# Performance work log

Measured on AMD Instinct MI355X. Metric: run time of the kernel, lower is better.

## Reference

```python
import jax, jax.numpy as jnp
import numpy as np

B, S, D, H = 4, 4096, 1024, 16
DH = D // H  # 64
EPS = 1e-6


def setup_inputs() -> dict:
    key = jax.random.key(0)
    ks = jax.random.split(key, 6)
    scale = 1.0 / np.sqrt(D).astype(np.float32)
    x = jax.random.normal(ks[0], (B, S, D), jnp.float32)
    # packed cache: rows 0..DH-1 = KV state S0, row DH = normalizer z0 (kept positive)
    state_cache = jax.random.uniform(ks[1], (B, H, DH + 1, DH), jnp.float32)
    Wq = jax.random.normal(ks[2], (D, D), jnp.float32) * scale
    Wk = jax.random.normal(ks[3], (D, D), jnp.float32) * scale
    Wv = jax.random.normal(ks[4], (D, D), jnp.float32) * scale
    Wo = jax.random.normal(ks[5], (D, D), jnp.float32) * scale
    return {"x": x, "state_cache": state_cache, "Wq": Wq, "Wk": Wk, "Wv": Wv, "Wo": Wo}


def reference(x, state_cache, Wq, Wk, Wv, Wo):
    b, s, d = x.shape
    h, dh = H, d // H

    def heads(t):  # [b,s,d] -> [s,b,h,dh] (seq-major for scan)
        return t.reshape(b, s, h, dh).transpose(1, 0, 2, 3)

    phi = lambda t: jax.nn.elu(t) + 1.0  # positive feature map
    q = phi(heads(x @ Wq))
    k = phi(heads(x @ Wk))
    v = heads(x @ Wv)

    S0 = state_cache[:, :, :dh, :]   # [b,h,dh,dh]
    z0 = state_cache[:, :, dh, :]    # [b,h,dh]

    def step(carry, inp):
        Sst, z = carry
        qt, kt, vt = inp  # each [b,h,dh]
        Sst = Sst + jnp.einsum('bhd,bhe->bhde', kt, vt)
        z = z + kt
        num = jnp.einsum('bhd,bhde->bhe', qt, Sst)            # [b,h,dh]
        den = jnp.einsum('bhd,bhd->bh', qt, z)[..., None]     # [b,h,1]
        return (Sst, z), num / (den + EPS)

    _, outs = jax.lax.scan(step, (S0, z0), (q, k, v))  # outs: [s,b,h,dh]
    out = outs.transpose(1, 0, 2, 3).reshape(b, s, d)
    return out @ Wo
```

## Files before the change

### kernel.cpp

```cpp
#include <hip/hip_runtime.h>

#define B_ 4
#define S_ 4096
#define D_ 1024
#define H_ 16
#define DH 64
#define CHUNK 64
#define NC (S_ / CHUNK)
#define BH (B_ * H_)
#define EPS 1e-6f

typedef __bf16 bf16;
typedef __bf16 bf16x8 __attribute__((ext_vector_type(8)));
typedef __bf16 bf16x4 __attribute__((ext_vector_type(4)));
typedef float v4f __attribute__((ext_vector_type(4)));

#define MFMA16(a, b, c) __builtin_amdgcn_mfma_f32_16x16x32_bf16(a, b, c, 0, 0, 0)

__device__ __forceinline__ void load_lds16(const bf16* g, bf16* l) {
  __builtin_amdgcn_global_load_lds(
      (const __attribute__((address_space(1))) unsigned int*)g,
      (__attribute__((address_space(3))) unsigned int*)l, 16, 0, 0);
}

__device__ __forceinline__ int swz72(int row, int col) {
  return row * 72 + ((((col >> 3) ^ (row >> 3)) & 7) << 3) + (col & 7);
}

__global__ __launch_bounds__(256) void cvt_f32_bf16(const float* __restrict__ in,
                                                    bf16* __restrict__ out) {
  const size_t i = ((size_t)blockIdx.x * 256 + threadIdx.x) * 8;
  float4 a = *(const float4*)(in + i);
  float4 b = *(const float4*)(in + i + 4);
  bf16x8 o;
  o[0] = (bf16)a.x; o[1] = (bf16)a.y; o[2] = (bf16)a.z; o[3] = (bf16)a.w;
  o[4] = (bf16)b.x; o[5] = (bf16)b.y; o[6] = (bf16)b.z; o[7] = (bf16)b.w;
  *(bf16x8*)(out + i) = o;
}

__global__ __launch_bounds__(256) void transpose_w4(
    const float* __restrict__ w0, const float* __restrict__ w1,
    const float* __restrict__ w2, const float* __restrict__ w3,
    bf16* __restrict__ out) {
  __shared__ float tile[32][33];
  const int z = blockIdx.z;
  const float* in = (z == 0) ? w0 : (z == 1) ? w1 : (z == 2) ? w2 : w3;
  bf16* o = out + (size_t)z * D_ * D_;
  const int bx = blockIdx.x * 32, by = blockIdx.y * 32;
  const int tx = threadIdx.x & 31, ty = threadIdx.x >> 5;
#pragma unroll
  for (int i = 0; i < 32; i += 8)
    tile[ty + i][tx] = in[(size_t)(by + ty + i) * D_ + bx + tx];
  __syncthreads();
#pragma unroll
  for (int i = 0; i < 32; i += 8)
    o[(size_t)(bx + ty + i) * D_ + by + tx] = (bf16)tile[tx][ty + i];
}

__global__ __launch_bounds__(256) void gemm_nt(const bf16* __restrict__ A,
                                               const bf16* __restrict__ BT,
                                               bf16* __restrict__ o0,
                                               bf16* __restrict__ o1,
                                               bf16* __restrict__ o2,
                                               float* __restrict__ of) {
  constexpr int TM = 128, BK = 32;
  constexpr int CLD = 132;
  __shared__ __align__(16) char smem[32768];
  float* Cl = (float*)smem;

  const int tid = threadIdx.x;
  const int wave = tid >> 6, lane = tid & 63;
  const int quad = lane >> 4, l16 = lane & 15;
  const int bm = blockIdx.x * TM;
  const int zz = blockIdx.y >> 3;
  const int colg = (blockIdx.y & 7) * 128;
  const int wm = (wave & 1) * 64, wn = (wave >> 1) * 64;
  const int act = (of == nullptr) && (zz < 2);
  bf16* ob = (zz == 0) ? o0 : (zz == 1) ? o1 : o2;

  const int srow = wave * 16 + (lane >> 2);
  const int sgrp = ((lane & 3) - ((lane >> 2) >> 1)) & 3;
  const bf16* gA0 = A + (size_t)(bm + srow) * D_ + sgrp * 8;
  const bf16* gA1 = gA0 + (size_t)64 * D_;
  const bf16* gB0 = BT + ((size_t)blockIdx.y * 128 + srow) * D_ + sgrp * 8;
  const bf16* gB1 = gB0 + (size_t)64 * D_;

  int offA[4], offB[4];
#pragma unroll
  for (int i = 0; i < 4; i++) {
    const int pg = (quad + (l16 >> 1)) & 3;
    offA[i] = (wm + i * 16 + l16) * BK + pg * 8;
    offB[i] = (wn + i * 16 + l16) * BK + pg * 8;
  }

  v4f zero = {0.f, 0.f, 0.f, 0.f};
  v4f acc[4][4];
#pragma unroll
  for (int i = 0; i < 4; i++)
#pragma unroll
    for (int j = 0; j < 4; j++) acc[i][j] = zero;

  auto stage = [&](int ks, int s) {
    bf16* As = (bf16*)(smem + s * 16384);
    bf16* Bs = As + 4096;
    const int ko = ks * BK;
    load_lds16(gA0 + ko, As + wave * 16 * BK);
    load_lds16(gA1 + ko, As + (64 + wave * 16) * BK);
    load_lds16(gB0 + ko, Bs + wave * 16 * BK);
    load_lds16(gB1 + ko, Bs + (64 + wave * 16) * BK);
  };
  auto compute = [&](int s) {
    const bf16* As = (const bf16*)(smem + s * 16384);
    const bf16* Bs = As + 4096;
    bf16x8 af[4], bfr[4];
#pragma unroll
    for (int i = 0; i < 4; i++) af[i] = *(const bf16x8*)&As[offA[i]];
#pragma unroll
    for (int j = 0; j < 4; j++) bfr[j] = *(const bf16x8*)&Bs[offB[j]];
#pragma unroll
    for (int i = 0; i < 4; i++)
#pragma unroll
      for (int j = 0; j < 4; j++) acc[i][j] = MFMA16(af[i], bfr[j], acc[i][j]);
  };

  constexpr int NK = D_ / BK;
  stage(0, 0);
  __syncthreads();
  for (int k = 0; k < NK; k += 2) {
    if (k + 1 < NK) stage(k + 1, 1);
    compute(0);
    __syncthreads();
    if (k + 2 < NK) stage(k + 2, 0);
    compute(1);
    __syncthreads();
  }

  const int lr = (wave & 1) * 16 + quad * 4;
  const int rrow = tid >> 3;
  const int rseg = (tid & 7) * 16;
  const int grow = bm + (rrow >> 4) * 64 + (rrow & 15);
#pragma unroll
  for (int i = 0; i < 4; i++) {
    __syncthreads();
#pragma unroll
    for (int j = 0; j < 4; j++) {
      const int col = wn + j * 16 + l16;
#pragma unroll
      for (int r = 0; r < 4; r++) {
        float x = acc[i][j][r];
        if (act) x = x > 0.f ? x + 1.f : __expf(x);
        Cl[(lr + r) * CLD + col] = x;
      }
    }
    __syncthreads();
    const float* src = &Cl[rrow * CLD + rseg];
    if (of) {
      float* dst = of + (size_t)(grow + i * 16) * D_ + colg + rseg;
#pragma unroll
      for (int u = 0; u < 4; u++)
        *(float4*)(dst + u * 4) = *(const float4*)(src + u * 4);
    } else {
      bf16x8 q0, q1;
#pragma unroll
      for (int u = 0; u < 8; u++) { q0[u] = (bf16)src[u]; q1[u] = (bf16)src[8 + u]; }
      bf16* dst = ob + (size_t)(grow + i * 16) * D_ + colg + rseg;
      *(bf16x8*)dst = q0;
      *(bf16x8*)(dst + 8) = q1;
    }
  }
}

__global__ __launch_bounds__(256) void chunk_kv(const bf16* __restrict__ kb,
                                                const bf16* __restrict__ vb,
                                                bf16* __restrict__ csum,
                                                float* __restrict__ zbuf) {
  __shared__ __align__(16) bf16 KT[DH * 72];
  __shared__ __align__(16) bf16 VT[DH * 72];
  const int tid = threadIdx.x;
  const int wave = tid >> 6, lane = tid & 63;
  const int quad = lane >> 4, l16 = lane & 15;
  const int c = blockIdx.x, bh = blockIdx.y;
  const int b = bh >> 4, h = bh & 15;
  const size_t gbase = ((size_t)(b * S_ + c * CHUNK)) * D_ + h * DH;
#pragma unroll
  for (int rep = 0; rep < 2; rep++) {
    int flat = tid + rep * 256;
    int r = flat >> 3, sg = (flat & 7) * 8;
    bf16x8 kk = *(const bf16x8*)(kb + gbase + (size_t)r * D_ + sg);
    bf16x8 vv = *(const bf16x8*)(vb + gbase + (size_t)r * D_ + sg);
#pragma unroll
    for (int u = 0; u < 8; u++) {
      KT[swz72(sg + u, r)] = kk[u];
      VT[swz72(sg + u, r)] = vv[u];
    }
  }
  __syncthreads();

  v4f zero = {0.f, 0.f, 0.f, 0.f};
  v4f acc[4];
#pragma unroll
  for (int j = 0; j < 4; j++) acc[j] = zero;
#pragma unroll
  for (int ks = 0; ks < 2; ks++) {
    bf16x8 ak = *(const bf16x8*)&KT[swz72(wave * 16 + l16, ks * 32 + quad * 8)];
#pragma unroll
    for (int j = 0; j < 4; j++) {
      bf16x8 bv = *(const bf16x8*)&VT[swz72(j * 16 + l16, ks * 32 + quad * 8)];
      acc[j] = MFMA16(ak, bv, acc[j]);
    }
  }
  bf16* out = csum + ((size_t)bh * NC + c) * 4096;
#pragma unroll
  for (int j = 0; j < 4; j++)
#pragma unroll
    for (int r = 0; r < 4; r++)
      out[(wave * 16 + quad * 4 + r) * 64 + (j * 16 + l16)] = (bf16)acc[j][r];

  {
    const int d = tid >> 2, p = tid & 3;
    bf16x8 a0 = *(const bf16x8*)&KT[swz72(d, p * 16)];
    bf16x8 a1 = *(const bf16x8*)&KT[swz72(d, p * 16 + 8)];
    float zp = 0.f;
#pragma unroll
    for (int u = 0; u < 8; u++) zp += (float)a0[u] + (float)a1[u];
    zp += __shfl_xor(zp, 1, 64);
    zp += __shfl_xor(zp, 2, 64);
    if (p == 0) zbuf[((size_t)bh * NC + c) * 64 + d] = zp;
  }
}

__global__ __launch_bounds__(256) void state_prefix(const float* __restrict__ sc,
                                                    const bf16* __restrict__ csum,
                                                    float* __restrict__ zbuf,
                                                    bf16* __restrict__ stb) {
  const int bh = blockIdx.x;
  const int e = blockIdx.y * 256 + threadIdx.x;
  const float* scb = sc + (size_t)bh * (DH + 1) * DH;
  if (e < 4096) {
    float run = scb[e];
    const bf16* p = csum + (size_t)bh * NC * 4096 + e;
    bf16* q = stb + (size_t)bh * NC * 4096 + e;
#pragma unroll 1
    for (int c = 0; c < NC; c += 4) {
      float t0 = (float)p[(size_t)(c + 0) * 4096];
      float t1 = (float)p[(size_t)(c + 1) * 4096];
      float t2 = (float)p[(size_t)(c + 2) * 4096];
      float t3 = (float)p[(size_t)(c + 3) * 4096];
      q[(size_t)(c + 0) * 4096] = (bf16)run; run += t0;
      q[(size_t)(c + 1) * 4096] = (bf16)run; run += t1;
      q[(size_t)(c + 2) * 4096] = (bf16)run; run += t2;
      q[(size_t)(c + 3) * 4096] = (bf16)run; run += t3;
    }
  } else if (e < 4160) {
    const int d = e - 4096;
    float run = scb[4096 + d];
    float* p = zbuf + (size_t)bh * NC * 64 + d;
#pragma unroll 1
    for (int c = 0; c < NC; c += 4) {
      float t0 = p[(size_t)(c + 0) * 64];
      float t1 = p[(size_t)(c + 1) * 64];
      float t2 = p[(size_t)(c + 2) * 64];
      float t3 = p[(size_t)(c + 3) * 64];
      p[(size_t)(c + 0) * 64] = run; run += t0;
      p[(size_t)(c + 1) * 64] = run; run += t1;
      p[(size_t)(c + 2) * 64] = run; run += t2;
      p[(size_t)(c + 3) * 64] = run; run += t3;
    }
  }
}

__global__ __launch_bounds__(256) void attn_pass2(
    const bf16* __restrict__ qb, const bf16* __restrict__ kb,
    const bf16* __restrict__ vb, const float* __restrict__ zbuf,
    const bf16* __restrict__ stb, bf16* __restrict__ ao) {
  __shared__ __align__(16) bf16 Ql[CHUNK * 72];
  __shared__ __align__(16) bf16 Kl[CHUNK * 72];
  __shared__ __align__(16) bf16 VT[DH * 72];
  __shared__ __align__(16) bf16 S0T[DH * 72];
  __shared__ __align__(16) bf16 Pl[CHUNK * 72];
  __shared__ float denl[CHUNK];
  __shared__ float z0l[DH];
  const int tid = threadIdx.x;
  const int wave = tid >> 6, lane = tid & 63;
  const int quad = lane >> 4, l16 = lane & 15;
  const int c = blockIdx.x, bh = blockIdx.y;
  const int b = bh >> 4, h = bh & 15;
  const size_t gbase = ((size_t)(b * S_ + c * CHUNK)) * D_ + h * DH;

#pragma unroll
  for (int rep = 0; rep < 2; rep++) {
    int flat = tid + rep * 256;
    int r = flat >> 3, sg = (flat & 7) * 8;
    *(bf16x8*)&Ql[swz72(r, sg)] = *(const bf16x8*)(qb + gbase + (size_t)r * D_ + sg);
    *(bf16x8*)&Kl[swz72(r, sg)] = *(const bf16x8*)(kb + gbase + (size_t)r * D_ + sg);
    bf16x8 vv = *(const bf16x8*)(vb + gbase + (size_t)r * D_ + sg);
#pragma unroll
    for (int u = 0; u < 8; u++) VT[swz72(sg + u, r)] = vv[u];
  }
  {
    const bf16* stb_c = stb + ((size_t)bh * NC + c) * 4096;
    const int f0 = tid * 16;
    const int col = f0 >> 6, row0 = f0 & 63;
    bf16x8 a0 = *(const bf16x8*)&stb_c[f0];
    bf16x8 a1 = *(const bf16x8*)&stb_c[f0 + 8];
#pragma unroll
    for (int u = 0; u < 8; u++) {
      S0T[swz72(row0 + u, col)] = a0[u];
      S0T[swz72(row0 + 8 + u, col)] = a1[u];
    }
  }
  if (tid < DH) z0l[tid] = zbuf[((size_t)bh * NC + c) * 64 + tid];
  __syncthreads();

  v4f zero = {0.f, 0.f, 0.f, 0.f};
  v4f pacc[4];
#pragma unroll
  for (int j = 0; j < 4; j++) pacc[j] = zero;
#pragma unroll
  for (int ks = 0; ks < 2; ks++) {
    bf16x8 aq = *(const bf16x8*)&Ql[swz72(wave * 16 + l16, ks * 32 + quad * 8)];
#pragma unroll
    for (int j = 0; j < 4; j++) {
      bf16x8 bk = *(const bf16x8*)&Kl[swz72(j * 16 + l16, ks * 32 + quad * 8)];
      pacc[j] = MFMA16(aq, bk, pacc[j]);
    }
  }
  float rs[4] = {0.f, 0.f, 0.f, 0.f};
#pragma unroll
  for (int j = 0; j < 4; j++) {
#pragma unroll
    for (int r = 0; r < 4; r++) {
      int t = wave * 16 + quad * 4 + r;
      int col = j * 16 + l16;
      float p = (col <= t) ? pacc[j][r] : 0.f;
      Pl[swz72(t, col)] = (bf16)p;
      rs[r] += p;
    }
  }
#pragma unroll
  for (int m = 1; m < 16; m <<= 1)
#pragma unroll
    for (int r = 0; r < 4; r++) rs[r] += __shfl_xor(rs[r], m, 64);
  if (l16 == 0)
#pragma unroll
    for (int r = 0; r < 4; r++) denl[wave * 16 + quad * 4 + r] = rs[r];
  __syncthreads();
  {
    const int t = tid >> 2, p = tid & 3;
    bf16x8 qa = *(const bf16x8*)&Ql[swz72(t, p * 16)];
    bf16x8 qb2 = *(const bf16x8*)&Ql[swz72(t, p * 16 + 8)];
    float qz = 0.f;
#pragma unroll
    for (int u = 0; u < 8; u++)
      qz += (float)qa[u] * z0l[p * 16 + u] + (float)qb2[u] * z0l[p * 16 + 8 + u];
    qz += __shfl_xor(qz, 1, 64);
    qz += __shfl_xor(qz, 2, 64);
    if (p == 0) denl[t] += qz;
  }
  __syncthreads();

  v4f nacc[4];
#pragma unroll
  for (int j = 0; j < 4; j++) nacc[j] = zero;
#pragma unroll
  for (int ks = 0; ks < 2; ks++) {
    bf16x8 ap = *(const bf16x8*)&Pl[swz72(wave * 16 + l16, ks * 32 + quad * 8)];
#pragma unroll
    for (int j = 0; j < 4; j++) {
      bf16x8 bv = *(const bf16x8*)&VT[swz72(j * 16 + l16, ks * 32 + quad * 8)];
      nacc[j] = MFMA16(ap, bv, nacc[j]);
    }
  }
#pragma unroll
  for (int ks = 0; ks < 2; ks++) {
    bf16x8 aq = *(const bf16x8*)&Ql[swz72(wave * 16 + l16, ks * 32 + quad * 8)];
#pragma unroll
    for (int j = 0; j < 4; j++) {
      bf16x8 bs = *(const bf16x8*)&S0T[swz72(j * 16 + l16, ks * 32 + quad * 8)];
      nacc[j] = MFMA16(aq, bs, nacc[j]);
    }
  }

  __syncthreads();
  bf16* Ol = Ql;
#pragma unroll
  for (int j = 0; j < 4; j++) {
#pragma unroll
    for (int r = 0; r < 4; r++) {
      int t = wave * 16 + quad * 4 + r;
      int e = j * 16 + l16;
      Ol[swz72(t, e)] = (bf16)(nacc[j][r] / (denl[t] + EPS));
    }
  }
  __syncthreads();
  {
    const int orow = tid >> 2, oc0 = (tid & 3) * 16;
    bf16x8 q0 = *(const bf16x8*)&Ol[swz72(orow, oc0)];
    bf16x8 q1 = *(const bf16x8*)&Ol[swz72(orow, oc0 + 8)];
    bf16* dst = ao + gbase + (size_t)orow * D_ + oc0;
    *(bf16x8*)dst = q0;
    *(bf16x8*)(dst + 8) = q1;
  }
}

extern "C" void kernel_launch(void* const* d_in, const int* in_sizes, int n_in,
                              void* d_out, int out_size, void* d_ws, size_t ws_size,
                              hipStream_t stream) {
  const float* x  = (const float*)d_in[0];
  const float* sc = (const float*)d_in[1];
  const float* Wq = (const float*)d_in[2];
  const float* Wk = (const float*)d_in[3];
  const float* Wv = (const float*)d_in[4];
  const float* Wo = (const float*)d_in[5];
  float* out = (float*)d_out;

  const size_t MSZ = (size_t)B_ * S_ * D_;
  const size_t WSZ = (size_t)D_ * D_;
  bf16* xb = (bf16*)d_ws;
  bf16* qb = xb + MSZ;
  bf16* kb = qb + MSZ;
  bf16* vb = kb + MSZ;
  bf16* ao = vb + MSZ;
  bf16* wt = ao + MSZ;
  bf16* csum = wt + 4 * WSZ;
  float* zbuf = (float*)(csum + (size_t)BH * NC * 4096);
  bf16* stb = xb;

  cvt_f32_bf16<<<MSZ / (256 * 8), 256, 0, stream>>>(x, xb);
  transpose_w4<<<dim3(32, 32, 4), 256, 0, stream>>>(Wq, Wk, Wv, Wo, wt);

  gemm_nt<<<dim3(128, 24), 256, 0, stream>>>(xb, wt, qb, kb, vb, nullptr);

  chunk_kv<<<dim3(NC, BH), 256, 0, stream>>>(kb, vb, csum, zbuf);
  state_prefix<<<dim3(BH, 17), 256, 0, stream>>>(sc, csum, zbuf, stb);
  attn_pass2<<<dim3(NC, BH), 256, 0, stream>>>(qb, kb, vb, zbuf, stb, ao);

  gemm_nt<<<dim3(128, 8), 256, 0, stream>>>(ao, wt + 3 * WSZ, nullptr, nullptr,
                                            nullptr, out);
}
```

Baseline: 387.6 us.

## Parallelize state prefix scan across chunks with LDS-tiled block scan

The chunk-state prefix kernel previously had each thread walk serially over all 64 chunks for one state element, using only 17 blocks per head with strided scalar bf16 loads. It now launches 64 blocks per head, each loading a 64-column by 64-chunk tile into shared memory with 16-byte vector loads. Four waves each scan 16 chunks, and their partial sums are combined in shared memory. Results are written back with vector stores, and the normalizer scan stays serial in a dedicated extra block. This exposes more parallelism and coalesces memory access, at the cost of extra synchronisation and shared memory.

```diff
diff --git a/kernel.cpp b/kernel.cpp
--- a/kernel.cpp
+++ b/kernel.cpp
@@ -12,7 +12,6 @@
 
 typedef __bf16 bf16;
 typedef __bf16 bf16x8 __attribute__((ext_vector_type(8)));
-typedef __bf16 bf16x4 __attribute__((ext_vector_type(4)));
 typedef float v4f __attribute__((ext_vector_type(4)));
 
 #define MFMA16(a, b, c) __builtin_amdgcn_mfma_f32_16x16x32_bf16(a, b, c, 0, 0, 0)
@@ -234,38 +233,60 @@
                                                     float* __restrict__ zbuf,
                                                     bf16* __restrict__ stb) {
   const int bh = blockIdx.x;
-  const int e = blockIdx.y * 256 + threadIdx.x;
+  const int g = blockIdx.y;
+  const int tid = threadIdx.x;
   const float* scb = sc + (size_t)bh * (DH + 1) * DH;
-  if (e < 4096) {
-    float run = scb[e];
-    const bf16* p = csum + (size_t)bh * NC * 4096 + e;
-    bf16* q = stb + (size_t)bh * NC * 4096 + e;
+  if (g == 64) {
+    if (tid < DH) {
+      const int d = tid;
+      float run = scb[4096 + d];
+      float* p = zbuf + (size_t)bh * NC * 64 + d;
 #pragma unroll 1
-    for (int c = 0; c < NC; c += 4) {
-      float t0 = (float)p[(size_t)(c + 0) * 4096];
-      float t1 = (float)p[(size_t)(c + 1) * 4096];
-      float t2 = (float)p[(size_t)(c + 2) * 4096];
-      float t3 = (float)p[(size_t)(c + 3) * 4096];
-      q[(size_t)(c + 0) * 4096] = (bf16)run; run += t0;
-      q[(size_t)(c + 1) * 4096] = (bf16)run; run += t1;
-      q[(size_t)(c + 2) * 4096] = (bf16)run; run += t2;
-      q[(size_t)(c + 3) * 4096] = (bf16)run; run += t3;
-    }
-  } else if (e < 4160) {
-    const int d = e - 4096;
-    float run = scb[4096 + d];
-    float* p = zbuf + (size_t)bh * NC * 64 + d;
-#pragma unroll 1
-    for (int c = 0; c < NC; c += 4) {
-      float t0 = p[(size_t)(c + 0) * 64];
-      float t1 = p[(size_t)(c + 1) * 64];
-      float t2 = p[(size_t)(c + 2) * 64];
-      float t3 = p[(size_t)(c + 3) * 64];
-      p[(size_t)(c + 0) * 64] = run; run += t0;
-      p[(size_t)(c + 1) * 64] = run; run += t1;
-      p[(size_t)(c + 2) * 64] = run; run += t2;
-      p[(size_t)(c + 3) * 64] = run; run += t3;
-    }
+      for (int c = 0; c < NC; c += 4) {
+        float t0 = p[(size_t)(c + 0) * 64];
+        float t1 = p[(size_t)(c + 1) * 64];
+        float t2 = p[(size_t)(c + 2) * 64];
+        float t3 = p[(size_t)(c + 3) * 64];
+        p[(size_t)(c + 0) * 64] = run; run += t0;
+        p[(size_t)(c + 1) * 64] = run; run += t1;
+        p[(size_t)(c + 2) * 64] = run; run += t2;
+        p[(size_t)(c + 3) * 64] = run; run += t3;
+      }
+    }
+    return;
+  }
+  __shared__ bf16 tile[NC][64];
+  __shared__ bf16 otile[NC][64];
+  __shared__ float partial[4][64];
+  const int x0 = g * 64;
+  const bf16* base = csum + (size_t)bh * NC * 4096 + x0;
+#pragma unroll
+  for (int rep = 0; rep < 2; rep++) {
+    int flat = tid + rep * 256;
+    int c = flat >> 3, seg = (flat & 7) * 8;
+    *(bf16x8*)&tile[c][seg] = *(const bf16x8*)(base + (size_t)c * 4096 + seg);
+  }
+  __syncthreads();
+  const int x = tid & 63, cq = tid >> 6, c0 = cq * 16;
+  float v[16];
+  float s = 0.f;
+#pragma unroll
+  for (int k = 0; k < 16; k++) { v[k] = (float)tile[c0 + k][x]; s += v[k]; }
+  partial[cq][x] = s;
+  __syncthreads();
+  float run = scb[x0 + x];
+#pragma unroll
+  for (int q = 0; q < 3; q++)
+    if (q < cq) run += partial[q][x];
+#pragma unroll
+  for (int k = 0; k < 16; k++) { otile[c0 + k][x] = (bf16)run; run += v[k]; }
+  __syncthreads();
+  bf16* obase = stb + (size_t)bh * NC * 4096 + x0;
+#pragma unroll
+  for (int rep = 0; rep < 2; rep++) {
+    int flat = tid + rep * 256;
+    int c = flat >> 3, seg = (flat & 7) * 8;
+    *(bf16x8*)(obase + (size_t)c * 4096 + seg) = *(const bf16x8*)&otile[c][seg];
   }
 }
 
@@ -432,7 +453,7 @@
   gemm_nt<<<dim3(128, 24), 256, 0, stream>>>(xb, wt, qb, kb, vb, nullptr);
 
   chunk_kv<<<dim3(NC, BH), 256, 0, stream>>>(kb, vb, csum, zbuf);
-  state_prefix<<<dim3(BH, 17), 256, 0, stream>>>(sc, csum, zbuf, stb);
+  state_prefix<<<dim3(BH, 65), 256, 0, stream>>>(sc, csum, zbuf, stb);
   attn_pass2<<<dim3(NC, BH), 256, 0, stream>>>(qb, kb, vb, zbuf, stb, ao);
 
   gemm_nt<<<dim3(128, 8), 256, 0, stream>>>(ao, wt + 3 * WSZ, nullptr, nullptr,
```

New measurement: 394.9 us. Within noise of the previous version (+1.9%).
